# Kernel tuning notes

Hardware: AMD Instinct MI355X
Metric: run time of the kernel (lower is better)

Reference implementation:

```python
import jax, jax.numpy as jnp
import numpy as np

B, T, F, H = 64, 2048, 64, 160


def setup_inputs() -> dict:
    key = jax.random.key(0)
    ks = jax.random.split(key, 20)
    s = lambda *shape: 0.05
    inp = {
        "x": jax.random.normal(ks[0], (B, T, F), jnp.float32),
        # dilated conv weight [out=F, in=F, k=3]
        "mix_w": jax.random.normal(ks[1], (F, F, 3), jnp.float32) * 0.1,
        # batchnorm (inference) params
        "bn_g": jnp.ones((F,), jnp.float32),
        "bn_b": jnp.zeros((F,), jnp.float32),
        "bn_m": jax.random.normal(ks[2], (F,), jnp.float32) * 0.1,
        "bn_v": jax.random.uniform(ks[3], (F,), jnp.float32, 0.5, 1.5),
        # GRU1: input F -> hidden H (pytorch gate order r, z, n)
        "w_ih1": jax.random.normal(ks[4], (3 * H, F), jnp.float32) * 0.05,
        "w_hh1": jax.random.normal(ks[5], (3 * H, H), jnp.float32) * 0.05,
        "b_ih1": jax.random.normal(ks[6], (3 * H,), jnp.float32) * 0.05,
        "b_hh1": jax.random.normal(ks[7], (3 * H,), jnp.float32) * 0.05,
        # GRU2: hidden H -> hidden H
        "w_ih2": jax.random.normal(ks[8], (3 * H, H), jnp.float32) * 0.05,
        "w_hh2": jax.random.normal(ks[9], (3 * H, H), jnp.float32) * 0.05,
        "b_ih2": jax.random.normal(ks[10], (3 * H,), jnp.float32) * 0.05,
        "b_hh2": jax.random.normal(ks[11], (3 * H,), jnp.float32) * 0.05,
        # head: Linear(H, H//2) -> GELU -> (dropout=identity in eval) -> Linear(H//2, 2)
        "hw1": jax.random.normal(ks[12], (H // 2, H), jnp.float32) * 0.05,
        "hb1": jnp.zeros((H // 2,), jnp.float32),
        "hw2": jax.random.normal(ks[13], (2, H // 2), jnp.float32) * 0.05,
        "hb2": jnp.zeros((2,), jnp.float32),
    }
    return inp


def _gru(z, w_ih, w_hh, b_ih, b_hh):
    # z: [B, T, in]; returns (all hidden states [B, T, H], final hidden [B, H])
    xg = jnp.einsum('bti,gi->btg', z, w_ih) + b_ih  # [B, T, 3H]
    xg = xg.transpose(1, 0, 2)                       # [T, B, 3H]
    h0 = jnp.zeros((z.shape[0], w_hh.shape[1]), z.dtype)

    def step(h, g):
        hg = h @ w_hh.T + b_hh
        xr, xz, xn = jnp.split(g, 3, axis=-1)
        hr, hz, hn = jnp.split(hg, 3, axis=-1)
        r = jax.nn.sigmoid(xr + hr)
        u = jax.nn.sigmoid(xz + hz)
        n = jnp.tanh(xn + r * hn)
        h_new = (1.0 - u) * n + u * h
        return h_new, h_new

    hT, hs = jax.lax.scan(step, h0, xg)
    return hs.transpose(1, 0, 2), hT


def reference(x, mix_w, bn_g, bn_b, bn_m, bn_v,
              w_ih1, w_hh1, b_ih1, b_hh1,
              w_ih2, w_hh2, b_ih2, b_hh2,
              hw1, hb1, hw2, hb2):
    # dilated conv over time: x [B,T,F] -> [B,F,T]
    xc = x.transpose(0, 2, 1)
    y = jax.lax.conv_general_dilated(
        xc, mix_w, window_strides=(1,), padding=[(2, 2)],
        rhs_dilation=(2,), dimension_numbers=('NCH', 'OIH', 'NCH'))
    # batchnorm (inference) + exact GELU
    scale = bn_g / jnp.sqrt(bn_v + 1e-5)
    y = (y - bn_m[:, None]) * scale[:, None] + bn_b[:, None]
    z = jax.nn.gelu(y, approximate=False).transpose(0, 2, 1)  # [B,T,F]

    h1, _ = _gru(z, w_ih1, w_hh1, b_ih1, b_hh1)    # [B,T,H]
    _, h2T = _gru(h1, w_ih2, w_hh2, b_ih2, b_hh2)  # [B,H] (last timestep)

    q = jax.nn.gelu(h2T @ hw1.T + hb1, approximate=False)
    return q @ hw2.T + hb2  # [B, 2]
```

## Files before the change

kernel.cpp:

```cpp
#include <hip/hip_runtime.h>
#include <cmath>

#define BB 64
#define TT 2048
#define FF 64
#define HH 160
#define G3 480
#define TC 128
#define NC (TT / TC)

#define L2E  1.44269504088896340736f
#define TL2E 2.88539008177792681472f

typedef unsigned int u32;
typedef _Float16 half8 __attribute__((ext_vector_type(8)));
typedef _Float16 half2v __attribute__((ext_vector_type(2)));
typedef float f32x4 __attribute__((ext_vector_type(4)));

__device__ __forceinline__ unsigned short f2h(float v) {
    _Float16 h = (_Float16)v;
    return __builtin_bit_cast(unsigned short, h);
}
__device__ __forceinline__ u32 packh2(float a, float b) {
    return (u32)f2h(a) | ((u32)f2h(b) << 16);
}
__device__ __forceinline__ u32 packhh(_Float16 a, _Float16 b) {
    return (u32)__builtin_bit_cast(unsigned short, a)
         | ((u32)__builtin_bit_cast(unsigned short, b) << 16);
}
__device__ __forceinline__ float h2lo(u32 p) {
    return (float)__builtin_bit_cast(half2v, p)[0];
}
__device__ __forceinline__ float h2hi(u32 p) {
    return (float)__builtin_bit_cast(half2v, p)[1];
}
__device__ __forceinline__ float h2sel(u32 p, u32 sh) {
    return (float)__builtin_bit_cast(half2v, p >> sh)[0];
}
__device__ __forceinline__ float frcp(float v) { return __builtin_amdgcn_rcpf(v); }
#if __has_builtin(__builtin_amdgcn_exp2f)
__device__ __forceinline__ float fexp2(float v) { return __builtin_amdgcn_exp2f(v); }
#else
__device__ __forceinline__ float fexp2(float v) { return __expf(v * 0.69314718055994530942f); }
#endif
__device__ __forceinline__ float gelu_exact(float v) {
    return 0.5f * v * (1.f + erff(v * 0.70710678118654752f));
}
__device__ __forceinline__ void barrier_lgkm() {
    asm volatile("s_waitcnt lgkmcnt(0)\ns_barrier" ::: "memory");
}
__device__ __forceinline__ half8 load_wrow8s(const float* p, float s) {
    const float4* q = (const float4*)p;
    float4 a = q[0], b = q[1];
    half8 r;
    r[0] = (_Float16)(a.x * s); r[1] = (_Float16)(a.y * s);
    r[2] = (_Float16)(a.z * s); r[3] = (_Float16)(a.w * s);
    r[4] = (_Float16)(b.x * s); r[5] = (_Float16)(b.y * s);
    r[6] = (_Float16)(b.z * s); r[7] = (_Float16)(b.w * s);
    return r;
}
__device__ __forceinline__ void split8(const float* v, half8& hi, half8& lo) {
    #pragma unroll
    for (int j = 0; j < 8; ++j) {
        _Float16 h = (_Float16)v[j];
        hi[j] = h;
        lo[j] = (_Float16)(v[j] - (float)h);
    }
}
#define MM16(A_, B_, C_) __builtin_amdgcn_mfma_f32_16x16x32_f16(A_, B_, C_, 0, 0, 0)

__global__ __launch_bounds__(256) void conv_mfma_kernel(
    const float* __restrict__ x, const float* __restrict__ mix_w,
    const float* __restrict__ bn_g, const float* __restrict__ bn_b,
    const float* __restrict__ bn_m, const float* __restrict__ bn_v,
    u32* __restrict__ z_out)
{
    __shared__ __align__(16) u32 xs[68 * 68];
    __shared__ __align__(8)  u32 zt[16 * 34];

    const int b   = blockIdx.y;
    const int t0  = blockIdx.x * 64;
    const int tid = threadIdx.x;
    const int wv = tid >> 6;
    const int lane = tid & 63;
    const int lane15 = lane & 15;
    const int quad = lane >> 4;

    {
        const float* xb = x + (size_t)b * TT * FF;
        for (int idx = tid; idx < 68 * 32; idx += 256) {
            const int row = idx >> 5;
            const int fp  = (idx & 31) * 2;
            const int t = t0 - 2 + row;
            float v0 = 0.f, v1 = 0.f;
            if (t >= 0 && t < TT) {
                float2 v = *(const float2*)(xb + (size_t)t * FF + fp);
                v0 = v.x; v1 = v.y;
            }
            _Float16 h0 = (_Float16)v0, h1 = (_Float16)v1;
            _Float16 l0 = (_Float16)(v0 - (float)h0);
            _Float16 l1 = (_Float16)(v1 - (float)h1);
            u32* rw = xs + row * 68;
            rw[(fp >> 1)]      = packhh(h0, h1);
            rw[32 + (fp >> 1)] = packhh(l0, l1);
        }
    }

    half8 Ahi[6], Alo[6];
    {
        const int fo = wv * 16 + lane15;
        const float* wrow = mix_w + fo * 192;
        #pragma unroll
        for (int s = 0; s < 6; ++s) {
            float wf[8];
            #pragma unroll
            for (int j = 0; j < 8; ++j) {
                int kap = s * 32 + quad * 8 + j;
                wf[j] = wrow[(kap & 63) * 3 + (kap >> 6)];
            }
            split8(wf, Ahi[s], Alo[s]);
        }
    }
    float sc[4], sh[4];
    #pragma unroll
    for (int r = 0; r < 4; ++r) {
        int f = wv * 16 + quad * 4 + r;
        float scl = bn_g[f] * rsqrtf(bn_v[f] + 1e-5f);
        sc[r] = scl; sh[r] = bn_b[f] - bn_m[f] * scl;
    }

    __syncthreads();

    u32* zrow = z_out + (size_t)(b >> 4) * TT * 512 + (b & 15) * 32;
    const int srow = tid >> 4;
    const int sc2  = tid & 15;

    for (int tt = 0; tt < 4; ++tt) {
        f32x4 C = {0.f, 0.f, 0.f, 0.f};
        #pragma unroll
        for (int s = 0; s < 6; ++s) {
            const int row = tt * 16 + lane15 + 2 * (s >> 1);
            const u32* rp = xs + row * 68 + (s & 1) * 16 + quad * 4;
            half8 Bhi = __builtin_bit_cast(half8, *(const uint4*)(rp));
            half8 Blo = __builtin_bit_cast(half8, *(const uint4*)(rp + 32));
            C = MM16(Ahi[s], Bhi, C);
            C = MM16(Ahi[s], Blo, C);
            C = MM16(Alo[s], Bhi, C);
        }
        float z0 = gelu_exact(fmaf(C[0], sc[0], sh[0]));
        float z1 = gelu_exact(fmaf(C[1], sc[1], sh[1]));
        float z2 = gelu_exact(fmaf(C[2], sc[2], sh[2]));
        float z3 = gelu_exact(fmaf(C[3], sc[3], sh[3]));
        const u32 q0 = packh2(z0, z1);
        const u32 q1 = packh2(z2, z3);
        __syncthreads();
        *(uint2*)(zt + lane15 * 34 + wv * 8 + quad * 2) = (uint2){q0, q1};
        __syncthreads();
        uint2 v = *(const uint2*)(zt + srow * 34 + sc2 * 2);
        *(uint2*)(zrow + (size_t)(t0 + tt * 16 + srow) * 512 + sc2 * 2) = v;
    }
}

#define DECLAI(i) half8 A##i##_0, A##i##_1, A##i##_2, A##i##_3, A##i##_4;
#define GLOADA(i) { int tl = wv4 + (i); int rowc = tl < 30 ? tl * 16 + lane15 : 479; \
    float sA = tl < 20 ? L2E : TL2E;                                                 \
    const float* wp = W + (size_t)rowc * K + quad * 8;                               \
    A##i##_0 = load_wrow8s(wp, sA); A##i##_1 = load_wrow8s(wp + 32, sA);             \
    if (KT > 2) { A##i##_2 = load_wrow8s(wp + 64, sA);                               \
                  A##i##_3 = load_wrow8s(wp + 96, sA);                               \
                  A##i##_4 = load_wrow8s(wp + 128, sA); }                            \
    else { A##i##_2 = A##i##_0; A##i##_3 = A##i##_0; A##i##_4 = A##i##_0; } }
#define GMM(i, kt) C##i = MM16(A##i##_##kt, Bk##kt, C##i);

template<int K, int KT, int TG>
__device__ __forceinline__ void gemm_body(
    const unsigned short* __restrict__ in,
    size_t in_blk_stride, int t_off,
    const float* __restrict__ W, const float* __restrict__ b_ih,
    const float* __restrict__ b_hh, u32* __restrict__ xg,
    int gidx, int tid)
{
    if (tid >= 512) return;
    const int wv4 = (tid >> 6) * 4;
    const int lane = tid & 63;
    const int lane15 = lane & 15;
    const int quad = lane >> 4;
    const int blk = gidx >> 4;
    const int tbase = (gidx & 15) * TG;

    DECLAI(0) DECLAI(1) DECLAI(2) DECLAI(3)
    GLOADA(0) GLOADA(1) GLOADA(2) GLOADA(3)

    f32x4 BIAS0, BIAS1, BIAS2, BIAS3;
    #define GBIAS(i) { int tl = wv4 + (i); int rowb = tl < 30 ? tl * 16 + quad * 4 : 476; \
        float sB = tl < 20 ? L2E : TL2E;                                                  \
        float4 bi = *(const float4*)(b_ih + rowb);                                        \
        if (tl < 20) { float4 bh = *(const float4*)(b_hh + rowb);                         \
            bi.x += bh.x; bi.y += bh.y; bi.z += bh.z; bi.w += bh.w; }                     \
        BIAS##i[0] = bi.x * sB; BIAS##i[1] = bi.y * sB;                                   \
        BIAS##i[2] = bi.z * sB; BIAS##i[3] = bi.w * sB; }
    GBIAS(0) GBIAS(1) GBIAS(2) GBIAS(3)
    #undef GBIAS

    const unsigned short* inb = in + (size_t)blk * in_blk_stride;
    u32* xgb = xg + (size_t)blk * TC * 3840;

    for (int t = 0; t < TG; ++t) {
        const int tt = tbase + t;
        const unsigned short* ip =
            inb + ((size_t)(t_off + tt) * 16 + lane15) * K + quad * 8;
        half8 Bk0 = __builtin_bit_cast(half8, *(const uint4*)(ip));
        half8 Bk1 = __builtin_bit_cast(half8, *(const uint4*)(ip + 32));
        half8 Bk2 = Bk0, Bk3 = Bk0, Bk4 = Bk0;
        if (KT > 2) {
            Bk2 = __builtin_bit_cast(half8, *(const uint4*)(ip + 64));
            Bk3 = __builtin_bit_cast(half8, *(const uint4*)(ip + 96));
            Bk4 = __builtin_bit_cast(half8, *(const uint4*)(ip + 128));
        }
        f32x4 C0 = BIAS0, C1 = BIAS1, C2 = BIAS2, C3 = BIAS3;
        GMM(0, 0) GMM(1, 0) GMM(2, 0) GMM(3, 0)
        GMM(0, 1) GMM(1, 1) GMM(2, 1) GMM(3, 1)
        if (KT > 2) {
            GMM(0, 2) GMM(1, 2) GMM(2, 2) GMM(3, 2)
            GMM(0, 3) GMM(1, 3) GMM(2, 3) GMM(3, 3)
            GMM(0, 4) GMM(1, 4) GMM(2, 4) GMM(3, 4)
        }
        #define GSTORE(i) { int tl = wv4 + (i); if (tl < 30) {                      \
            u32 q0 = packh2(C##i[0], C##i[1]);                                      \
            u32 q1 = packh2(C##i[2], C##i[3]);                                      \
            *(uint2*)(xgb + (((size_t)tt * 30 + tl) * 16 + lane15) * 8 + quad * 2)  \
                = (uint2){q0, q1}; } }
        GSTORE(0) GSTORE(1) GSTORE(2) GSTORE(3)
        #undef GSTORE
    }
}

#define DECLW(nm) half8 nm##0, nm##1, nm##2, nm##3, nm##4;
#define LOADWHS(nm, tb, S) { const float* wp = w_hh + (size_t)((tb) * 16 + lane15) * HH + quad * 8; \
    nm##0 = load_wrow8s(wp, S);       nm##1 = load_wrow8s(wp + 32, S);                              \
    nm##2 = load_wrow8s(wp + 64, S);  nm##3 = load_wrow8s(wp + 96, S);                              \
    nm##4 = load_wrow8s(wp + 128, S); }

template<bool WRITE_H>
__device__ __forceinline__ void scan_body(
    const u32* __restrict__ xg,
    const float* __restrict__ w_hh, const float* __restrict__ b_hh,
    float* __restrict__ h_state,
    u32* __restrict__ h_out32,
    int first, int blk, int sub, int tid, u32* h_lds32)
{
    const int wv = tid >> 6;
    const int lane = tid & 63;
    const int lane15 = lane & 15;
    const int quad = lane >> 4;
    const int ch   = lane15 & 3;
    const int dup  = lane15 >> 2;
    const int ch0  = sub * 4;
    const int row_g = wv * 16 + quad * 4 + dup;
    const u32 shamt = (u32)(16 * (dup & 1));
    const bool d1 = (dup & 1) != 0;
    const bool d2 = (dup & 2) != 0;

    DECLW(Ar) DECLW(Az) DECLW(An)
    LOADWHS(Ar, wv, L2E) LOADWHS(Az, 10 + wv, L2E) LOADWHS(An, 20 + wv, TL2E)

    const float bh = b_hh[320 + row_g] * TL2E;

    float* hsp = h_state + (size_t)(blk * 16 + ch0 + ch) * HH + row_g;
    float ho = first ? 0.f : *hsp;

    const int widx = ch * 168 + row_g;
    unsigned short* hw16 = (unsigned short*)h_lds32;
    unsigned short* HW0 = hw16 + widx;
    unsigned short* HW1 = hw16 + 672 + widx;
    *HW0 = f2h(ho);

    const int vb = ch * 21 + quad;

    const u32* xgb = xg + (size_t)blk * TC * 3840;
    const int pr = quad * 2 + (dup >> 1);
    const int xo_r = ((wv)      * 16 + ch0 + ch) * 8 + pr;
    const int xo_z = ((10 + wv) * 16 + ch0 + ch) * 8 + pr;
    const int xo_n = ((20 + wv) * 16 + ch0 + ch) * 8 + pr;

    u32 xrP0 = xgb[0 * 3840 + xo_r], xzP0 = xgb[0 * 3840 + xo_z], xnP0 = xgb[0 * 3840 + xo_n];
    u32 xrP1 = xgb[1 * 3840 + xo_r], xzP1 = xgb[1 * 3840 + xo_z], xnP1 = xgb[1 * 3840 + xo_n];
    u32 xrP2 = xgb[2 * 3840 + xo_r], xzP2 = xgb[2 * 3840 + xo_z], xnP2 = xgb[2 * 3840 + xo_n];
    u32 xrP3 = xgb[3 * 3840 + xo_r], xzP3 = xgb[3 * 3840 + xo_z], xnP3 = xgb[3 * 3840 + xo_n];
    const u32* pf_r = xgb + 4 * 3840 + xo_r;
    const u32* pf_z = xgb + 4 * 3840 + xo_z;
    const u32* pf_n = xgb + 4 * 3840 + xo_n;

    unsigned short* hp = WRITE_H
            ? (unsigned short*)h_out32 + (size_t)blk * TC * 2560
              + (size_t)(ch0 + ch) * 160 + row_g
            : nullptr;
    __syncthreads();

    #define SCAN_STEP(RBOFF, HWP, XR, XZ, XN, PFO, HPO)                              \
    {                                                                                \
        const uint4* hb = (const uint4*)(h_lds32 + (RBOFF));                         \
        uint4 b0 = hb[vb];      uint4 b1 = hb[vb + 4];                               \
        uint4 b2 = hb[vb + 8];  uint4 b3 = hb[vb + 12];                              \
        uint4 b4 = hb[vb + 16];                                                      \
        float xrv = h2sel(XR, shamt);                                                \
        float xzv = h2sel(XZ, shamt);                                                \
        float xnv = h2sel(XN, shamt);                                                \
        f32x4 Cr = {xrv, xrv, xrv, xrv};                                             \
        f32x4 Cz = {xzv, xzv, xzv, xzv};                                             \
        f32x4 Cn = {bh, bh, bh, bh};                                                 \
        XR = pf_r[PFO]; XZ = pf_z[PFO]; XN = pf_n[PFO];                              \
        half8 B0 = __builtin_bit_cast(half8, b0);                                    \
        Cr = MM16(Ar0, B0, Cr); Cz = MM16(Az0, B0, Cz); Cn = MM16(An0, B0, Cn);      \
        half8 B1 = __builtin_bit_cast(half8, b1);                                    \
        Cr = MM16(Ar1, B1, Cr); Cz = MM16(Az1, B1, Cz); Cn = MM16(An1, B1, Cn);      \
        half8 B2 = __builtin_bit_cast(half8, b2);                                    \
        Cr = MM16(Ar2, B2, Cr); Cz = MM16(Az2, B2, Cz); Cn = MM16(An2, B2, Cn);      \
        half8 B3 = __builtin_bit_cast(half8, b3);                                    \
        Cr = MM16(Ar3, B3, Cr); Cz = MM16(Az3, B3, Cz); Cn = MM16(An3, B3, Cn);      \
        half8 B4 = __builtin_bit_cast(half8, b4);                                    \
        Cr = MM16(Ar4, B4, Cr); Cz = MM16(Az4, B4, Cz); Cn = MM16(An4, B4, Cn);      \
        {                                                                            \
            float ca = d1 ? Cr[1] : Cr[0];                                           \
            float cb = d1 ? Cr[3] : Cr[2];                                           \
            float crv = d2 ? cb : ca;                                                \
            ca = d1 ? Cz[1] : Cz[0];                                                 \
            cb = d1 ? Cz[3] : Cz[2];                                                 \
            float czv = d2 ? cb : ca;                                                \
            ca = d1 ? Cn[1] : Cn[0];                                                 \
            cb = d1 ? Cn[3] : Cn[2];                                                 \
            float cnv = d2 ? cb : ca;                                                \
            float r = frcp(1.f + fexp2(-crv));                                       \
            float u = frcp(1.f + fexp2(-czv));                                       \
            float e = fexp2(fmaf(r, cnv, xnv));                                      \
            float n = fmaf(-2.f, frcp(e + 1.f), 1.f);                                \
            ho = fmaf(u, ho - n, n);                                                 \
        }                                                                            \
        const unsigned short hv = f2h(ho);                                           \
        *(HWP) = hv;                                                                 \
        if (WRITE_H) { hp[HPO] = hv; }                                               \
        barrier_lgkm();                                                              \
    }

    for (int t4 = 0; t4 < TC; t4 += 4) {
        SCAN_STEP(0,   HW1, xrP0, xzP0, xnP0, 0 * 3840, 0 * 2560)
        SCAN_STEP(336, HW0, xrP1, xzP1, xnP1, 1 * 3840, 1 * 2560)
        SCAN_STEP(0,   HW1, xrP2, xzP2, xnP2, 2 * 3840, 2 * 2560)
        SCAN_STEP(336, HW0, xrP3, xzP3, xnP3, 3 * 3840, 3 * 2560)
        pf_r += 4 * 3840; pf_z += 4 * 3840; pf_n += 4 * 3840;
        if (WRITE_H) hp += 4 * 2560;
    }
    #undef SCAN_STEP

    *hsp = ho;
}

__global__ __launch_bounds__(640, 1) void pipe_stage(
    const u32* __restrict__ z,
    u32* __restrict__ xg1,
    u32* __restrict__ xg2,
    u32* __restrict__ h1c,
    float* __restrict__ h1s, float* __restrict__ h2s,
    const float* __restrict__ w_ih1, const float* __restrict__ b_ih1,
    const float* __restrict__ w_hh1, const float* __restrict__ b_hh1,
    const float* __restrict__ w_ih2, const float* __restrict__ b_ih2,
    const float* __restrict__ w_hh2, const float* __restrict__ b_hh2,
    int k)
{
    __shared__ __align__(16) u32 h_lds32[2 * 336];
    const int bx = blockIdx.x;
    const int tid = threadIdx.x;
    const size_t XGCH = (size_t)4 * TC * 3840;
    const size_t H1CH = (size_t)4 * TC * 1280;

    if (bx < 16) {
        const int c = k - 1;
        if (c < 0 || c >= NC) return;
        scan_body<true>(xg1 + (c & 1) * XGCH, w_hh1, b_hh1, h1s,
                        h1c + (c & 1) * H1CH, c == 0, bx >> 2, bx & 3, tid, h_lds32);
    } else if (bx < 32) {
        const int c = k - 3;
        if (c < 0 || c >= NC) return;
        scan_body<false>(xg2 + (c & 1) * XGCH, w_hh2, b_hh2, h2s,
                         nullptr, c == 0, (bx - 16) >> 2, (bx - 16) & 3, tid, h_lds32);
    } else if (bx < 96) {
        const int c = k;
        if (c >= NC) return;
        gemm_body<64, 2, 8>((const unsigned short*)z, (size_t)TT * 1024, c * TC,
                            w_ih1, b_ih1, b_hh1, xg1 + (c & 1) * XGCH, bx - 32, tid);
    } else {
        const int c = k - 2;
        if (c < 0 || c >= NC) return;
        gemm_body<160, 5, 8>((const unsigned short*)(h1c + (c & 1) * H1CH),
                             (size_t)TC * 2560, 0,
                             w_ih2, b_ih2, b_hh2, xg2 + (c & 1) * XGCH, bx - 96, tid);
    }
}

__global__ __launch_bounds__(256) void head_kernel(
    const float* __restrict__ h_state,
    const float* __restrict__ hw1, const float* __restrict__ hb1,
    const float* __restrict__ hw2, const float* __restrict__ hb2,
    float* __restrict__ out)
{
    const int b = blockIdx.x;
    const int tid = threadIdx.x;
    __shared__ float hf[HH];
    __shared__ float q[80];
    if (tid < HH) hf[tid] = h_state[b * HH + tid];
    __syncthreads();
    if (tid < 80) {
        float a = hb1[tid];
        const float* wr = hw1 + (size_t)tid * HH;
        #pragma unroll 8
        for (int i = 0; i < HH; ++i) a = fmaf(wr[i], hf[i], a);
        q[tid] = gelu_exact(a);
    }
    __syncthreads();
    if (tid < 2) {
        float o = hb2[tid];
        const float* wr = hw2 + tid * 80;
        #pragma unroll 8
        for (int j = 0; j < 80; ++j) o = fmaf(wr[j], q[j], o);
        out[b * 2 + tid] = o;
    }
}

extern "C" void kernel_launch(void* const* d_in, const int* in_sizes, int n_in,
                              void* d_out, int out_size, void* d_ws, size_t ws_size,
                              hipStream_t stream)
{
    const float* x     = (const float*)d_in[0];
    const float* mix_w = (const float*)d_in[1];
    const float* bn_g  = (const float*)d_in[2];
    const float* bn_b  = (const float*)d_in[3];
    const float* bn_m  = (const float*)d_in[4];
    const float* bn_v  = (const float*)d_in[5];
    const float* w_ih1 = (const float*)d_in[6];
    const float* w_hh1 = (const float*)d_in[7];
    const float* b_ih1 = (const float*)d_in[8];
    const float* b_hh1 = (const float*)d_in[9];
    const float* w_ih2 = (const float*)d_in[10];
    const float* w_hh2 = (const float*)d_in[11];
    const float* b_ih2 = (const float*)d_in[12];
    const float* b_hh2 = (const float*)d_in[13];
    const float* hw1   = (const float*)d_in[14];
    const float* hb1   = (const float*)d_in[15];
    const float* hw2   = (const float*)d_in[16];
    const float* hb2   = (const float*)d_in[17];
    float* out = (float*)d_out;

    char* p = (char*)d_ws;
    u32* z_ws  = (u32*)p;  p += (size_t)BB * TT * 32 * 4;
    u32* xg1_ws = (u32*)p; p += (size_t)2 * 4 * TC * 3840 * 4;
    u32* xg2_ws = (u32*)p; p += (size_t)2 * 4 * TC * 3840 * 4;
    u32* h1c_ws = (u32*)p; p += (size_t)2 * 4 * TC * 1280 * 4;
    float* h1s = (float*)p; p += (size_t)BB * HH * 4;
    float* h2s = (float*)p;

    conv_mfma_kernel<<<dim3(32, BB), 256, 0, stream>>>(
        x, mix_w, bn_g, bn_b, bn_m, bn_v, z_ws);

    for (int k = 0; k <= NC + 2; ++k) {
        pipe_stage<<<160, 640, 0, stream>>>(
            z_ws, xg1_ws, xg2_ws, h1c_ws, h1s, h2s,
            w_ih1, b_ih1, w_hh1, b_hh1,
            w_ih2, b_ih2, w_hh2, b_hh2, k);
    }

    head_kernel<<<BB, 256, 0, stream>>>(h2s, hw1, hb1, hw2, hb2, out);
}
```

Measured before the change: 1.615 ms.

## Give each scan wave two hidden-row tiles and shrink pipeline blocks to 512 threads

The GRU scan now assigns two 16-row tiles of the recurrent weights to each of 5 waves, down from one tile across 10 waves. Each wave issues 30 MFMAs per step and reuses each h fragment loaded from LDS twice, with fewer waves joining the per-step barrier. The block size drops from 640 to 512; the spare waves in scan blocks only mirror the barriers. The cost is about twice the weight registers per wave and a longer serial MFMA chain per step, and the other block roles now run with fewer threads.

```diff
diff --git a/kernel.cpp b/kernel.cpp
--- a/kernel.cpp
+++ b/kernel.cpp
@@ -27,12 +27,6 @@
 __device__ __forceinline__ u32 packhh(_Float16 a, _Float16 b) {
     return (u32)__builtin_bit_cast(unsigned short, a)
          | ((u32)__builtin_bit_cast(unsigned short, b) << 16);
-}
-__device__ __forceinline__ float h2lo(u32 p) {
-    return (float)__builtin_bit_cast(half2v, p)[0];
-}
-__device__ __forceinline__ float h2hi(u32 p) {
-    return (float)__builtin_bit_cast(half2v, p)[1];
 }
 __device__ __forceinline__ float h2sel(u32 p, u32 sh) {
     return (float)__builtin_bit_cast(half2v, p >> sh)[0];
@@ -48,6 +42,11 @@
 }
 __device__ __forceinline__ void barrier_lgkm() {
     asm volatile("s_waitcnt lgkmcnt(0)\ns_barrier" ::: "memory");
+}
+__device__ __forceinline__ float csel(f32x4 C, bool d1, bool d2) {
+    float ca = d1 ? C[1] : C[0];
+    float cb = d1 ? C[3] : C[2];
+    return d2 ? cb : ca;
 }
 __device__ __forceinline__ half8 load_wrow8s(const float* p, float s) {
     const float4* q = (const float4*)p;
@@ -249,6 +248,11 @@
     u32* __restrict__ h_out32,
     int first, int blk, int sub, int tid, u32* h_lds32)
 {
+    if (tid >= 320) {
+        __syncthreads();
+        for (int t = 0; t < TC; ++t) barrier_lgkm();
+        return;
+    }
     const int wv = tid >> 6;
     const int lane = tid & 63;
     const int lane15 = lane & 15;
@@ -256,106 +260,135 @@
     const int ch   = lane15 & 3;
     const int dup  = lane15 >> 2;
     const int ch0  = sub * 4;
-    const int row_g = wv * 16 + quad * 4 + dup;
-    const u32 shamt = (u32)(16 * (dup & 1));
+    const int row0 = 32 * wv + quad * 4 + dup;
+    const int row1 = row0 + 16;
+    const u32 shamt = 16u * (u32)(dup & 1);
     const bool d1 = (dup & 1) != 0;
     const bool d2 = (dup & 2) != 0;
 
-    DECLW(Ar) DECLW(Az) DECLW(An)
-    LOADWHS(Ar, wv, L2E) LOADWHS(Az, 10 + wv, L2E) LOADWHS(An, 20 + wv, TL2E)
-
-    const float bh = b_hh[320 + row_g] * TL2E;
-
-    float* hsp = h_state + (size_t)(blk * 16 + ch0 + ch) * HH + row_g;
-    float ho = first ? 0.f : *hsp;
-
-    const int widx = ch * 168 + row_g;
-    unsigned short* hw16 = (unsigned short*)h_lds32;
-    unsigned short* HW0 = hw16 + widx;
-    unsigned short* HW1 = hw16 + 672 + widx;
-    *HW0 = f2h(ho);
-
-    const int vb = ch * 21 + quad;
+    DECLW(Ra) DECLW(Rb) DECLW(Za) DECLW(Zb) DECLW(Na) DECLW(Nb)
+    LOADWHS(Ra, 2 * wv, L2E)      LOADWHS(Rb, 2 * wv + 1, L2E)
+    LOADWHS(Za, 10 + 2 * wv, L2E) LOADWHS(Zb, 11 + 2 * wv, L2E)
+    LOADWHS(Na, 20 + 2 * wv, TL2E) LOADWHS(Nb, 21 + 2 * wv, TL2E)
+
+    const float bh0 = b_hh[320 + row0] * TL2E;
+    const float bh1 = b_hh[320 + row1] * TL2E;
+
+    float* hsp = h_state + (size_t)(blk * 16 + ch0 + ch) * HH;
+    float ho0 = 0.f, ho1 = 0.f;
+    if (!first) { ho0 = hsp[row0]; ho1 = hsp[row1]; }
+
+    unsigned short* hb16 = (unsigned short*)h_lds32;
+    unsigned short* W0 = hb16 + ch * 208;
+    unsigned short* W1 = W0 + 832;
+    W0[row0] = f2h(ho0);
+    W0[row1] = f2h(ho1);
+
+    const int vb = ch * 26 + quad;
 
     const u32* xgb = xg + (size_t)blk * TC * 3840;
     const int pr = quad * 2 + (dup >> 1);
-    const int xo_r = ((wv)      * 16 + ch0 + ch) * 8 + pr;
-    const int xo_z = ((10 + wv) * 16 + ch0 + ch) * 8 + pr;
-    const int xo_n = ((20 + wv) * 16 + ch0 + ch) * 8 + pr;
-
-    u32 xrP0 = xgb[0 * 3840 + xo_r], xzP0 = xgb[0 * 3840 + xo_z], xnP0 = xgb[0 * 3840 + xo_n];
-    u32 xrP1 = xgb[1 * 3840 + xo_r], xzP1 = xgb[1 * 3840 + xo_z], xnP1 = xgb[1 * 3840 + xo_n];
-    u32 xrP2 = xgb[2 * 3840 + xo_r], xzP2 = xgb[2 * 3840 + xo_z], xnP2 = xgb[2 * 3840 + xo_n];
-    u32 xrP3 = xgb[3 * 3840 + xo_r], xzP3 = xgb[3 * 3840 + xo_z], xnP3 = xgb[3 * 3840 + xo_n];
-    const u32* pf_r = xgb + 4 * 3840 + xo_r;
-    const u32* pf_z = xgb + 4 * 3840 + xo_z;
-    const u32* pf_n = xgb + 4 * 3840 + xo_n;
+    const int xo = ((2 * wv) * 16 + ch0 + ch) * 8 + pr;
+
+    u32 r0A = xgb[0 * 3840 + xo],        r1A = xgb[0 * 3840 + xo + 128];
+    u32 z0A = xgb[0 * 3840 + xo + 1280], z1A = xgb[0 * 3840 + xo + 1408];
+    u32 n0A = xgb[0 * 3840 + xo + 2560], n1A = xgb[0 * 3840 + xo + 2688];
+    u32 r0B = xgb[1 * 3840 + xo],        r1B = xgb[1 * 3840 + xo + 128];
+    u32 z0B = xgb[1 * 3840 + xo + 1280], z1B = xgb[1 * 3840 + xo + 1408];
+    u32 n0B = xgb[1 * 3840 + xo + 2560], n1B = xgb[1 * 3840 + xo + 2688];
+    u32 r0C = xgb[2 * 3840 + xo],        r1C = xgb[2 * 3840 + xo + 128];
+    u32 z0C = xgb[2 * 3840 + xo + 1280], z1C = xgb[2 * 3840 + xo + 1408];
+    u32 n0C = xgb[2 * 3840 + xo + 2560], n1C = xgb[2 * 3840 + xo + 2688];
+    u32 r0D = xgb[3 * 3840 + xo],        r1D = xgb[3 * 3840 + xo + 128];
+    u32 z0D = xgb[3 * 3840 + xo + 1280], z1D = xgb[3 * 3840 + xo + 1408];
+    u32 n0D = xgb[3 * 3840 + xo + 2560], n1D = xgb[3 * 3840 + xo + 2688];
+    const u32* pf = xgb + 4 * 3840 + xo;
 
     unsigned short* hp = WRITE_H
             ? (unsigned short*)h_out32 + (size_t)blk * TC * 2560
-              + (size_t)(ch0 + ch) * 160 + row_g
+              + (size_t)(ch0 + ch) * 160 + row0
             : nullptr;
     __syncthreads();
 
-    #define SCAN_STEP(RBOFF, HWP, XR, XZ, XN, PFO, HPO)                              \
+    #define SCAN_STEP(RBOFF, WP, Xr0, Xr1, Xz0, Xz1, Xn0, Xn1, PFO, HPO)             \
     {                                                                                \
-        const uint4* hb = (const uint4*)(h_lds32 + (RBOFF));                         \
-        uint4 b0 = hb[vb];      uint4 b1 = hb[vb + 4];                               \
-        uint4 b2 = hb[vb + 8];  uint4 b3 = hb[vb + 12];                              \
-        uint4 b4 = hb[vb + 16];                                                      \
-        float xrv = h2sel(XR, shamt);                                                \
-        float xzv = h2sel(XZ, shamt);                                                \
-        float xnv = h2sel(XN, shamt);                                                \
-        f32x4 Cr = {xrv, xrv, xrv, xrv};                                             \
-        f32x4 Cz = {xzv, xzv, xzv, xzv};                                             \
-        f32x4 Cn = {bh, bh, bh, bh};                                                 \
-        XR = pf_r[PFO]; XZ = pf_z[PFO]; XN = pf_n[PFO];                              \
-        half8 B0 = __builtin_bit_cast(half8, b0);                                    \
-        Cr = MM16(Ar0, B0, Cr); Cz = MM16(Az0, B0, Cz); Cn = MM16(An0, B0, Cn);      \
-        half8 B1 = __builtin_bit_cast(half8, b1);                                    \
-        Cr = MM16(Ar1, B1, Cr); Cz = MM16(Az1, B1, Cz); Cn = MM16(An1, B1, Cn);      \
-        half8 B2 = __builtin_bit_cast(half8, b2);                                    \
-        Cr = MM16(Ar2, B2, Cr); Cz = MM16(Az2, B2, Cz); Cn = MM16(An2, B2, Cn);      \
-        half8 B3 = __builtin_bit_cast(half8, b3);                                    \
-        Cr = MM16(Ar3, B3, Cr); Cz = MM16(Az3, B3, Cz); Cn = MM16(An3, B3, Cn);      \
-        half8 B4 = __builtin_bit_cast(half8, b4);                                    \
-        Cr = MM16(Ar4, B4, Cr); Cz = MM16(Az4, B4, Cz); Cn = MM16(An4, B4, Cn);      \
+        const uint4* hb = (const uint4*)h_lds32 + (RBOFF);                           \
+        uint4 hq0 = hb[vb];      uint4 hq1 = hb[vb + 4];                             \
+        uint4 hq2 = hb[vb + 8];  uint4 hq3 = hb[vb + 12];                            \
+        uint4 hq4 = hb[vb + 16];                                                     \
+        float xr0v = h2sel(Xr0, shamt), xr1v = h2sel(Xr1, shamt);                    \
+        float xz0v = h2sel(Xz0, shamt), xz1v = h2sel(Xz1, shamt);                    \
+        float xn0v = h2sel(Xn0, shamt), xn1v = h2sel(Xn1, shamt);                    \
+        f32x4 Cr0 = {xr0v, xr0v, xr0v, xr0v}, Cr1 = {xr1v, xr1v, xr1v, xr1v};        \
+        f32x4 Cz0 = {xz0v, xz0v, xz0v, xz0v}, Cz1 = {xz1v, xz1v, xz1v, xz1v};        \
+        f32x4 Cn0 = {bh0, bh0, bh0, bh0},     Cn1 = {bh1, bh1, bh1, bh1};            \
+        Xr0 = pf[(PFO)];        Xr1 = pf[(PFO) + 128];                               \
+        Xz0 = pf[(PFO) + 1280]; Xz1 = pf[(PFO) + 1408];                              \
+        Xn0 = pf[(PFO) + 2560]; Xn1 = pf[(PFO) + 2688];                              \
+        half8 Bx;                                                                    \
+        Bx = __builtin_bit_cast(half8, hq0);                                         \
+        Cr0 = MM16(Ra0, Bx, Cr0); Cr1 = MM16(Rb0, Bx, Cr1);                          \
+        Cz0 = MM16(Za0, Bx, Cz0); Cz1 = MM16(Zb0, Bx, Cz1);                          \
+        Cn0 = MM16(Na0, Bx, Cn0); Cn1 = MM16(Nb0, Bx, Cn1);                          \
+        Bx = __builtin_bit_cast(half8, hq1);                                         \
+        Cr0 = MM16(Ra1, Bx, Cr0); Cr1 = MM16(Rb1, Bx, Cr1);                          \
+        Cz0 = MM16(Za1, Bx, Cz0); Cz1 = MM16(Zb1, Bx, Cz1);                          \
+        Cn0 = MM16(Na1, Bx, Cn0); Cn1 = MM16(Nb1, Bx, Cn1);                          \
+        Bx = __builtin_bit_cast(half8, hq2);                                         \
+        Cr0 = MM16(Ra2, Bx, Cr0); Cr1 = MM16(Rb2, Bx, Cr1);                          \
+        Cz0 = MM16(Za2, Bx, Cz0); Cz1 = MM16(Zb2, Bx, Cz1);                          \
+        Cn0 = MM16(Na2, Bx, Cn0); Cn1 = MM16(Nb2, Bx, Cn1);                          \
+        Bx = __builtin_bit_cast(half8, hq3);                                         \
+        Cr0 = MM16(Ra3, Bx, Cr0); Cr1 = MM16(Rb3, Bx, Cr1);                          \
+        Cz0 = MM16(Za3, Bx, Cz0); Cz1 = MM16(Zb3, Bx, Cz1);                          \
+        Cn0 = MM16(Na3, Bx, Cn0); Cn1 = MM16(Nb3, Bx, Cn1);                          \
+        Bx = __builtin_bit_cast(half8, hq4);                                         \
+        Cr0 = MM16(Ra4, Bx, Cr0); Cr1 = MM16(Rb4, Bx, Cr1);                          \
+        Cz0 = MM16(Za4, Bx, Cz0); Cz1 = MM16(Zb4, Bx, Cz1);                          \
+        Cn0 = MM16(Na4, Bx, Cn0); Cn1 = MM16(Nb4, Bx, Cn1);                          \
         {                                                                            \
-            float ca = d1 ? Cr[1] : Cr[0];                                           \
-            float cb = d1 ? Cr[3] : Cr[2];                                           \
-            float crv = d2 ? cb : ca;                                                \
-            ca = d1 ? Cz[1] : Cz[0];                                                 \
-            cb = d1 ? Cz[3] : Cz[2];                                                 \
-            float czv = d2 ? cb : ca;                                                \
-            ca = d1 ? Cn[1] : Cn[0];                                                 \
-            cb = d1 ? Cn[3] : Cn[2];                                                 \
-            float cnv = d2 ? cb : ca;                                                \
+            float crv = csel(Cr0, d1, d2);                                           \
+            float czv = csel(Cz0, d1, d2);                                           \
+            float cnv = csel(Cn0, d1, d2);                                           \
             float r = frcp(1.f + fexp2(-crv));                                       \
             float u = frcp(1.f + fexp2(-czv));                                       \
-            float e = fexp2(fmaf(r, cnv, xnv));                                      \
+            float e = fexp2(fmaf(r, cnv, xn0v));                                     \
             float n = fmaf(-2.f, frcp(e + 1.f), 1.f);                                \
-            ho = fmaf(u, ho - n, n);                                                 \
+            ho0 = fmaf(u, ho0 - n, n);                                               \
         }                                                                            \
-        const unsigned short hv = f2h(ho);                                           \
-        *(HWP) = hv;                                                                 \
-        if (WRITE_H) { hp[HPO] = hv; }                                               \
+        {                                                                            \
+            float crv = csel(Cr1, d1, d2);                                           \
+            float czv = csel(Cz1, d1, d2);                                           \
+            float cnv = csel(Cn1, d1, d2);                                           \
+            float r = frcp(1.f + fexp2(-crv));                                       \
+            float u = frcp(1.f + fexp2(-czv));                                       \
+            float e = fexp2(fmaf(r, cnv, xn1v));                                     \
+            float n = fmaf(-2.f, frcp(e + 1.f), 1.f);                                \
+            ho1 = fmaf(u, ho1 - n, n);                                               \
+        }                                                                            \
+        const unsigned short hv0 = f2h(ho0);                                         \
+        const unsigned short hv1 = f2h(ho1);                                         \
+        (WP)[row0] = hv0;                                                            \
+        (WP)[row1] = hv1;                                                            \
+        if (WRITE_H) { hp[(HPO)] = hv0; hp[(HPO) + 16] = hv1; }                      \
         barrier_lgkm();                                                              \
     }
 
     for (int t4 = 0; t4 < TC; t4 += 4) {
-        SCAN_STEP(0,   HW1, xrP0, xzP0, xnP0, 0 * 3840, 0 * 2560)
-        SCAN_STEP(336, HW0, xrP1, xzP1, xnP1, 1 * 3840, 1 * 2560)
-        SCAN_STEP(0,   HW1, xrP2, xzP2, xnP2, 2 * 3840, 2 * 2560)
-        SCAN_STEP(336, HW0, xrP3, xzP3, xnP3, 3 * 3840, 3 * 2560)
-        pf_r += 4 * 3840; pf_z += 4 * 3840; pf_n += 4 * 3840;
+        SCAN_STEP(0,   W1, r0A, r1A, z0A, z1A, n0A, n1A, 0 * 3840, 0 * 2560)
+        SCAN_STEP(104, W0, r0B, r1B, z0B, z1B, n0B, n1B, 1 * 3840, 1 * 2560)
+        SCAN_STEP(0,   W1, r0C, r1C, z0C, z1C, n0C, n1C, 2 * 3840, 2 * 2560)
+        SCAN_STEP(104, W0, r0D, r1D, z0D, z1D, n0D, n1D, 3 * 3840, 3 * 2560)
+        pf += 4 * 3840;
         if (WRITE_H) hp += 4 * 2560;
     }
     #undef SCAN_STEP
 
-    *hsp = ho;
-}
-
-__global__ __launch_bounds__(640, 1) void pipe_stage(
+    hsp[row0] = ho0;
+    hsp[row1] = ho1;
+}
+
+__global__ __launch_bounds__(512, 1) void pipe_stage(
     const u32* __restrict__ z,
     u32* __restrict__ xg1,
     u32* __restrict__ xg2,
@@ -367,7 +400,7 @@
     const float* __restrict__ w_hh2, const float* __restrict__ b_hh2,
     int k)
 {
-    __shared__ __align__(16) u32 h_lds32[2 * 336];
+    __shared__ __align__(16) u32 h_lds32[2 * 416];
     const int bx = blockIdx.x;
     const int tid = threadIdx.x;
     const size_t XGCH = (size_t)4 * TC * 3840;
@@ -462,7 +495,7 @@
         x, mix_w, bn_g, bn_b, bn_m, bn_v, z_ws);
 
     for (int k = 0; k <= NC + 2; ++k) {
-        pipe_stage<<<160, 640, 0, stream>>>(
+        pipe_stage<<<160, 512, 0, stream>>>(
             z_ws, xg1_ws, xg2_ws, h1c_ws, h1s, h2s,
             w_ih1, b_ih1, w_hh1, b_hh1,
             w_ih2, b_ih2, w_hh2, b_hh2, k);
```

Result: slower. 1.953 ms (+21.0%).
